# Kernel tuning notes

Hardware: AMD Instinct MI355X
Metric: run time of the kernel (lower is better)

Reference implementation:

```python
import jax, jax.numpy as jnp
import numpy as np

N_NODES = 50000
N_NEIB = 64
D = 256
BATCH = 1024
N_SAMPLES = (25, 10)  # fanout per layer (layer_specs n_sample)


def setup_inputs() -> dict:
    key = jax.random.key(0)
    ks = jax.random.split(key, 12)
    inp = {
        'ids': jax.random.randint(ks[0], (BATCH,), 0, N_NODES),
        'diff_idx': jax.random.randint(ks[1], (N_NODES, N_NEIB), 0, N_NODES),
        'diff_val': jax.random.uniform(ks[2], (N_NODES, N_NEIB), dtype=jnp.float32),
        'feats': jax.random.normal(ks[3], (N_NODES, D), dtype=jnp.float32),
    }
    # two aggregator layers, each: fc_x, fc_neib : D -> D (= output_dim//2)
    for li in range(2):
        inp[f'Wx{li+1}'] = jax.random.normal(ks[4 + 4 * li], (D, D), dtype=jnp.float32) * 0.05
        inp[f'bx{li+1}'] = jnp.zeros((D,), dtype=jnp.float32)
        inp[f'Wn{li+1}'] = jax.random.normal(ks[5 + 4 * li], (D, D), dtype=jnp.float32) * 0.05
        inp[f'bn{li+1}'] = jnp.zeros((D,), dtype=jnp.float32)
    return inp


def _sample(diff_idx, diff_val, ids, n_samples, key):
    # gather candidate neighbor rows, shared random column permutation, take first n_samples
    tmp_idx = diff_idx[ids]            # [n, N_NEIB]
    tmp_val = diff_val[ids]
    perm = jax.random.permutation(key, tmp_idx.shape[1])
    idx = tmp_idx[:, perm][:, :n_samples].reshape(-1)
    val = tmp_val[:, perm][:, :n_samples].reshape(-1)
    return idx, val


def _agg(x, neib, vals, Wx, bx, Wn, bn):
    # weighted-mean neighbor aggregation + self/neib linear combine + relu
    n = x.shape[0]
    d = neib.shape[1]
    neib = neib.reshape(n, -1, d)              # [n, s, d]
    vals = vals.reshape(n, -1)                 # [n, s]
    w = vals / (jnp.sum(vals, axis=1, keepdims=True) + 1e-10)
    m = jnp.einsum('nsd,ns->nd', neib, w)      # weighted mean of neighbors
    return jax.nn.relu(x @ Wx + bx + m @ Wn + bn)


def reference(ids, diff_idx, diff_val, feats,
              Wx1, bx1, Wn1, bn1, Wx2, bx2, Wn2, bn2):
    skey = jax.random.key(42)
    all_feats = [feats[ids]]
    all_vals = []
    cur = ids
    for li, n in enumerate(N_SAMPLES):
        cur, vals = _sample(diff_idx, diff_val, cur, n, jax.random.fold_in(skey, li))
        all_feats.append(feats[cur])
        all_vals.append(vals)
    params = [(Wx1, bx1, Wn1, bn1), (Wx2, bx2, Wn2, bn2)]
    for Wx, bx, Wn, bn in params:
        all_feats = [_agg(all_feats[k], all_feats[k + 1], all_vals[k], Wx, bx, Wn, bn)
                     for k in range(len(all_feats) - 1)]
    assert len(all_feats) == 1
    return all_feats[0]  # [BATCH, D]
```

## Files before the change

kernel.cpp:

```cpp
#include <hip/hip_runtime.h>
#include <stdint.h>
#include <stddef.h>
#include <algorithm>

#define BATCH  1024
#define S1     25
#define S2     10
#define DIM    256
#define NNEIB  64
#define L2ROWS (BATCH * S1)
#define MROWS  (BATCH + BATCH * S1)
#define KTOT   512
#define NFEAT  50000

struct Perm25 { int p[S1]; };
struct Perm10 { int p[S2]; };

typedef __attribute__((ext_vector_type(8))) short short8;
typedef __attribute__((ext_vector_type(4))) float f32x4;

static inline uint32_t rotl_(uint32_t x, int d) { return (x << d) | (x >> (32 - d)); }

static void tf2x32(uint32_t k0, uint32_t k1, uint32_t x0, uint32_t x1,
                   uint32_t* o0, uint32_t* o1) {
  const uint32_t ks0 = k0, ks1 = k1, ks2 = k0 ^ k1 ^ 0x1BD11BDAu;
  static const int R[8] = {13, 15, 26, 6, 17, 29, 16, 24};
  x0 += ks0; x1 += ks1;
  for (int g = 0; g < 5; ++g) {
    const int* rr = R + (g & 1) * 4;
    for (int i = 0; i < 4; i++) { x0 += x1; x1 = rotl_(x1, rr[i]); x1 ^= x0; }
    uint32_t a, b;
    switch (g) {
      default:
      case 0: a = ks1; b = ks2; break;
      case 1: a = ks2; b = ks0; break;
      case 2: a = ks0; b = ks1; break;
      case 3: a = ks1; b = ks2; break;
      case 4: a = ks2; b = ks0; break;
    }
    x0 += a; x1 = x1 + b + (uint32_t)(g + 1);
  }
  *o0 = x0; *o1 = x1;
}

static void compute_perm(uint32_t li, int n, int* out) {
  uint32_t k0, k1, s0, s1;
  tf2x32(0u, 42u, 0u, li, &k0, &k1);
  tf2x32(k0, k1, 0u, 1u, &s0, &s1);
  uint32_t bits[NNEIB];
  for (int i = 0; i < NNEIB; i++) {
    uint32_t a, b;
    tf2x32(s0, s1, 0u, (uint32_t)i, &a, &b);
    bits[i] = a ^ b;
  }
  int idx[NNEIB];
  for (int i = 0; i < NNEIB; i++) idx[i] = i;
  std::stable_sort(idx, idx + NNEIB, [&](int A, int B) { return bits[A] < bits[B]; });
  for (int j = 0; j < n; j++) out[j] = idx[j];
}

__device__ __forceinline__ unsigned short f2bf(float x) {
  union { float f; uint32_t u; } v; v.f = x;
  uint32_t r = (v.u + 0x7FFFu + ((v.u >> 16) & 1u)) >> 16;
  return (unsigned short)r;
}
__device__ __forceinline__ float bfbits2f(uint32_t lo16) {
  union { uint32_t u; float f; } v; v.u = lo16 << 16;
  return v.f;
}


__global__ __launch_bounds__(256) void convf_k(
    const float* __restrict__ feats, uint32_t* __restrict__ fb) {
  int i = blockIdx.x * 256 + threadIdx.x;
  f32x4 v = *(const f32x4*)&feats[(size_t)i * 4];
  uint32_t lo = f2bf(v.x) | ((uint32_t)f2bf(v.y) << 16);
  uint32_t hi = f2bf(v.z) | ((uint32_t)f2bf(v.w) << 16);
  fb[(size_t)i * 2]     = lo;
  fb[(size_t)i * 2 + 1] = hi;
}

__global__ __launch_bounds__(256) void sample1_k(
    const int* __restrict__ ids, const int* __restrict__ dix,
    const float* __restrict__ dval, int* __restrict__ growB,
    float* __restrict__ w1, Perm25 pm) {
  int i = blockIdx.x * 256 + threadIdx.x;
  if (i >= BATCH) return;
  int nid = ids[i];
  growB[i] = nid;
  const float* vr = dval + (size_t)nid * NNEIB;
  const int* ir = dix + (size_t)nid * NNEIB;
  float v[S1];
  float s = 0.f;
  for (int j = 0; j < S1; j++) { v[j] = vr[pm.p[j]]; s += v[j]; }
  float inv = 1.f / (s + 1e-10f);
  for (int j = 0; j < S1; j++) {
    w1[i * S1 + j] = v[j] * inv;
    growB[BATCH + i * S1 + j] = ir[pm.p[j]];
  }
}

__global__ __launch_bounds__(256) void sample2_k(
    const int* __restrict__ idx1, const int* __restrict__ dix,
    const float* __restrict__ dval, int* __restrict__ idx2,
    float* __restrict__ w2, Perm10 pm) {
  int p = blockIdx.x * 256 + threadIdx.x;
  if (p >= L2ROWS) return;
  int nid = idx1[p];
  const float* vr = dval + (size_t)nid * NNEIB;
  const int* ir = dix + (size_t)nid * NNEIB;
  float v[S2];
  float s = 0.f;
  for (int j = 0; j < S2; j++) { v[j] = vr[pm.p[j]]; s += v[j]; }
  float inv = 1.f / (s + 1e-10f);
  for (int j = 0; j < S2; j++) {
    w2[p * S2 + j] = v[j] * inv;
    idx2[p * S2 + j] = ir[pm.p[j]];
  }
}

__global__ __launch_bounds__(256) void stage1_k(
    const uint2* __restrict__ fb, const int* __restrict__ growB,
    const int* __restrict__ idx1, const float* __restrict__ w1,
    const int* __restrict__ idx2, const float* __restrict__ w2,
    uint2* __restrict__ A1) {
  int wave = threadIdx.x >> 6, lane = threadIdx.x & 63;
  int r = blockIdx.x * 4 + wave;
  int s;
  const int* nb;
  const float* ww;
  if (r < BATCH) { s = S1; nb = idx1 + (size_t)r * S1; ww = w1 + (size_t)r * S1; }
  else { s = S2; int b = r - BATCH; nb = idx2 + (size_t)b * S2; ww = w2 + (size_t)b * S2; }
  int nbl = 0;
  float wl = 0.f;
  if (lane < s) { nbl = nb[lane]; wl = ww[lane]; }
  int xrow = growB[r];
  A1[(size_t)r * 128 + lane] = fb[(size_t)xrow * 64 + lane];
  float a0 = 0.f, a1 = 0.f, a2 = 0.f, a3 = 0.f;
  for (int j = 0; j < s; j++) {
    int nid = __shfl(nbl, j);
    float wj = __shfl(wl, j);
    uint2 u = fb[(size_t)nid * 64 + lane];
    a0 += wj * bfbits2f(u.x & 0xffffu);
    a1 += wj * bfbits2f(u.x >> 16);
    a2 += wj * bfbits2f(u.y & 0xffffu);
    a3 += wj * bfbits2f(u.y >> 16);
  }
  uint2 o;
  o.x = f2bf(a0) | ((uint32_t)f2bf(a1) << 16);
  o.y = f2bf(a2) | ((uint32_t)f2bf(a3) << 16);
  A1[(size_t)r * 128 + 64 + lane] = o;
}

__global__ __launch_bounds__(256) void stage2_k(
    const uint2* __restrict__ Hb, const float* __restrict__ w1,
    uint2* __restrict__ A2) {
  int wave = threadIdx.x >> 6, lane = threadIdx.x & 63;
  int i = blockIdx.x * 4 + wave;
  float wl = (lane < S1) ? w1[(size_t)i * S1 + lane] : 0.f;
  A2[(size_t)i * 128 + lane] = Hb[(size_t)i * 64 + lane];
  const uint2* hb = Hb + (size_t)(BATCH + i * S1) * 64 + lane;
  float a0 = 0.f, a1 = 0.f, a2 = 0.f, a3 = 0.f;
  for (int j = 0; j < S1; j++) {
    float wj = __shfl(wl, j);
    uint2 u = hb[(size_t)j * 64];
    a0 += wj * bfbits2f(u.x & 0xffffu);
    a1 += wj * bfbits2f(u.x >> 16);
    a2 += wj * bfbits2f(u.y & 0xffffu);
    a3 += wj * bfbits2f(u.y >> 16);
  }
  uint2 o;
  o.x = f2bf(a0) | ((uint32_t)f2bf(a1) << 16);
  o.y = f2bf(a2) | ((uint32_t)f2bf(a3) << 16);
  A2[(size_t)i * 128 + 64 + lane] = o;
}

__global__ __launch_bounds__(256) void convw_k(
    const float* __restrict__ Wx, const float* __restrict__ Wn,
    unsigned short* __restrict__ Wt) {
  int idx = blockIdx.x * 256 + threadIdx.x;
  int n = idx >> 9;
  int k = idx & 511;
  float v = (k < DIM) ? Wx[(size_t)k * DIM + n] : Wn[(size_t)(k - DIM) * DIM + n];
  Wt[(size_t)n * KTOT + k] = f2bf(v);
}

#define BK 32
#define LPAD 40
template <int TBM, int TBN, bool OUT_BF16>
__global__ __launch_bounds__(256) void gemm_k(
    const unsigned short* __restrict__ A, const unsigned short* __restrict__ Wt,
    const float* __restrict__ bx, const float* __restrict__ bn,
    void* __restrict__ OutP) {
  constexpr int MI = TBM / 32;
  constexpr int NJ = TBN / 32;
  __shared__ __align__(16) unsigned short As[TBM][LPAD];
  __shared__ __align__(16) unsigned short Bs[TBN][LPAD];
  int t = threadIdx.x;
  int wave = t >> 6, lane = t & 63, quad = lane >> 4, l16 = lane & 15;
  int wm = (wave >> 1) * (TBM / 2);
  int wn = (wave & 1) * (TBN / 2);
  int row0 = blockIdx.x * TBM, col0 = blockIdx.y * TBN;

  f32x4 acc[MI][NJ];
#pragma unroll
  for (int i = 0; i < MI; i++)
#pragma unroll
    for (int j = 0; j < NJ; j++) acc[i][j] = (f32x4){0.f, 0.f, 0.f, 0.f};

  int lr = t >> 2;
  int lq = (t & 3) * 8;

  for (int k0 = 0; k0 < KTOT; k0 += BK) {
#pragma unroll
    for (int p = 0; p < TBM / 64; p++)
      *(f32x4*)&As[p * 64 + lr][lq] =
          *(const f32x4*)&A[(size_t)(row0 + p * 64 + lr) * KTOT + k0 + lq];
#pragma unroll
    for (int p = 0; p < TBN / 64; p++)
      *(f32x4*)&Bs[p * 64 + lr][lq] =
          *(const f32x4*)&Wt[(size_t)(col0 + p * 64 + lr) * KTOT + k0 + lq];
    __syncthreads();

    short8 af[MI], bfr[NJ];
#pragma unroll
    for (int i = 0; i < MI; i++)
      af[i] = *(const short8*)&As[wm + i * 16 + l16][quad * 8];
#pragma unroll
    for (int j = 0; j < NJ; j++)
      bfr[j] = *(const short8*)&Bs[wn + j * 16 + l16][quad * 8];
#pragma unroll
    for (int i = 0; i < MI; i++)
#pragma unroll
      for (int j = 0; j < NJ; j++)
        acc[i][j] = __builtin_amdgcn_mfma_f32_16x16x32_bf16(af[i], bfr[j], acc[i][j], 0, 0, 0);
    __syncthreads();
  }

  float bias[NJ];
#pragma unroll
  for (int j = 0; j < NJ; j++) {
    int c = col0 + wn + j * 16 + l16;
    bias[j] = bx[c] + bn[c];
  }
#pragma unroll
  for (int i = 0; i < MI; i++) {
#pragma unroll
    for (int j = 0; j < NJ; j++) {
      int c = col0 + wn + j * 16 + l16;
#pragma unroll
      for (int reg = 0; reg < 4; reg++) {
        int r = row0 + wm + i * 16 + quad * 4 + reg;
        float v = fmaxf(acc[i][j][reg] + bias[j], 0.f);
        if (OUT_BF16)
          ((unsigned short*)OutP)[(size_t)r * DIM + c] = f2bf(v);
        else
          ((float*)OutP)[(size_t)r * DIM + c] = v;
      }
    }
  }
}

static inline size_t align256(size_t x) { return (x + 255) & ~(size_t)255; }

extern "C" void kernel_launch(void* const* d_in, const int* in_sizes, int n_in,
                              void* d_out, int out_size, void* d_ws, size_t ws_size,
                              hipStream_t stream) {
  const int*   ids  = (const int*)d_in[0];
  const int*   dix  = (const int*)d_in[1];
  const float* dval = (const float*)d_in[2];
  const float* feats= (const float*)d_in[3];
  const float* Wx1  = (const float*)d_in[4];
  const float* bx1  = (const float*)d_in[5];
  const float* Wn1  = (const float*)d_in[6];
  const float* bn1  = (const float*)d_in[7];
  const float* Wx2  = (const float*)d_in[8];
  const float* bx2  = (const float*)d_in[9];
  const float* Wn2  = (const float*)d_in[10];
  const float* bn2  = (const float*)d_in[11];
  float* out = (float*)d_out;

  Perm25 p25;
  Perm10 p10;
  compute_perm(0u, S1, p25.p);
  compute_perm(1u, S2, p10.p);

  char* w = (char*)d_ws;
  int*            growB = (int*)w;            w += align256(sizeof(int) * MROWS);
  float*          w1    = (float*)w;          w += align256(sizeof(float) * L2ROWS);
  int*            idx2  = (int*)w;            w += align256(sizeof(int) * (size_t)L2ROWS * S2);
  float*          w2    = (float*)w;          w += align256(sizeof(float) * (size_t)L2ROWS * S2);
  uint32_t*       fb    = (uint32_t*)w;       w += align256(2 * (size_t)NFEAT * DIM);
  unsigned short* A1    = (unsigned short*)w; w += align256(2 * (size_t)MROWS * KTOT);
  unsigned short* Hb    = (unsigned short*)w; w += align256(2 * (size_t)MROWS * DIM);
  unsigned short* A2    = (unsigned short*)w; w += align256(2 * (size_t)BATCH * KTOT);
  unsigned short* Wt1   = (unsigned short*)w; w += align256(2 * (size_t)DIM * KTOT);
  unsigned short* Wt2   = (unsigned short*)w; w += align256(2 * (size_t)DIM * KTOT);
  int* idx1 = growB + BATCH;

  convf_k<<<(NFEAT * DIM / 4) / 256, 256, 0, stream>>>(feats, fb);
  convw_k<<<(DIM * KTOT) / 256, 256, 0, stream>>>(Wx1, Wn1, Wt1);
  convw_k<<<(DIM * KTOT) / 256, 256, 0, stream>>>(Wx2, Wn2, Wt2);
  sample1_k<<<(BATCH + 255) / 256, 256, 0, stream>>>(ids, dix, dval, growB, w1, p25);
  sample2_k<<<(L2ROWS + 255) / 256, 256, 0, stream>>>(idx1, dix, dval, idx2, w2, p10);
  stage1_k<<<MROWS / 4, 256, 0, stream>>>((const uint2*)fb, growB, idx1, w1, idx2, w2,
                                          (uint2*)A1);
  gemm_k<128, 128, true><<<dim3(MROWS / 128, DIM / 128), 256, 0, stream>>>(
      A1, Wt1, bx1, bn1, Hb);
  stage2_k<<<BATCH / 4, 256, 0, stream>>>((const uint2*)Hb, w1, (uint2*)A2);
  gemm_k<64, 64, false><<<dim3(BATCH / 64, DIM / 64), 256, 0, stream>>>(
      A2, Wt2, bx2, bn2, out);
}
```

Baseline: 202.2 us.

## Merge prep kernels, fold layer-2 sampling into stage1, gather self rows in GEMM

Combines the feature conversion, both weight conversions and layer-1 sampling into one prep kernel. Layer-2 sampling moves into stage1, which computes the normalized weights with a wave shuffle, so idx2/w2 are never written. The GEMMs now read the self rows straight from the bf16 feature table (or Hb) through an index, so the concatenated A matrices with their copied self halves are gone. This removes launches and intermediate traffic, at the cost of indirect row loads in the GEMM A-tile path.

```diff
diff --git a/kernel.cpp b/kernel.cpp
--- a/kernel.cpp
+++ b/kernel.cpp
@@ -70,72 +70,74 @@
 }
 
 
-__global__ __launch_bounds__(256) void convf_k(
-    const float* __restrict__ feats, uint32_t* __restrict__ fb) {
-  int i = blockIdx.x * 256 + threadIdx.x;
-  f32x4 v = *(const f32x4*)&feats[(size_t)i * 4];
-  uint32_t lo = f2bf(v.x) | ((uint32_t)f2bf(v.y) << 16);
-  uint32_t hi = f2bf(v.z) | ((uint32_t)f2bf(v.w) << 16);
-  fb[(size_t)i * 2]     = lo;
-  fb[(size_t)i * 2 + 1] = hi;
-}
-
-__global__ __launch_bounds__(256) void sample1_k(
+#define PREP_CONVF   12500
+#define PREP_CONVW   512
+#define PREP_BLOCKS  (PREP_CONVF + 2 * PREP_CONVW + 4)
+__global__ __launch_bounds__(256) void prep_k(
+    const float* __restrict__ feats, uint32_t* __restrict__ fb,
+    const float* __restrict__ Wx1, const float* __restrict__ Wn1,
+    unsigned short* __restrict__ Wt1,
+    const float* __restrict__ Wx2, const float* __restrict__ Wn2,
+    unsigned short* __restrict__ Wt2,
     const int* __restrict__ ids, const int* __restrict__ dix,
-    const float* __restrict__ dval, int* __restrict__ growB,
+    const float* __restrict__ dval, int* __restrict__ idx1,
     float* __restrict__ w1, Perm25 pm) {
-  int i = blockIdx.x * 256 + threadIdx.x;
-  if (i >= BATCH) return;
-  int nid = ids[i];
-  growB[i] = nid;
-  const float* vr = dval + (size_t)nid * NNEIB;
-  const int* ir = dix + (size_t)nid * NNEIB;
-  float v[S1];
-  float s = 0.f;
-  for (int j = 0; j < S1; j++) { v[j] = vr[pm.p[j]]; s += v[j]; }
-  float inv = 1.f / (s + 1e-10f);
-  for (int j = 0; j < S1; j++) {
-    w1[i * S1 + j] = v[j] * inv;
-    growB[BATCH + i * S1 + j] = ir[pm.p[j]];
-  }
-}
-
-__global__ __launch_bounds__(256) void sample2_k(
-    const int* __restrict__ idx1, const int* __restrict__ dix,
-    const float* __restrict__ dval, int* __restrict__ idx2,
-    float* __restrict__ w2, Perm10 pm) {
-  int p = blockIdx.x * 256 + threadIdx.x;
-  if (p >= L2ROWS) return;
-  int nid = idx1[p];
-  const float* vr = dval + (size_t)nid * NNEIB;
-  const int* ir = dix + (size_t)nid * NNEIB;
-  float v[S2];
-  float s = 0.f;
-  for (int j = 0; j < S2; j++) { v[j] = vr[pm.p[j]]; s += v[j]; }
-  float inv = 1.f / (s + 1e-10f);
-  for (int j = 0; j < S2; j++) {
-    w2[p * S2 + j] = v[j] * inv;
-    idx2[p * S2 + j] = ir[pm.p[j]];
+  int b = blockIdx.x, t = threadIdx.x;
+  if (b < PREP_CONVF) {
+    int i = b * 256 + t;
+    f32x4 v = *(const f32x4*)&feats[(size_t)i * 4];
+    fb[(size_t)i * 2]     = f2bf(v.x) | ((uint32_t)f2bf(v.y) << 16);
+    fb[(size_t)i * 2 + 1] = f2bf(v.z) | ((uint32_t)f2bf(v.w) << 16);
+  } else if (b < PREP_CONVF + 2 * PREP_CONVW) {
+    int wi = b - PREP_CONVF;
+    const float* Wx = (wi < PREP_CONVW) ? Wx1 : Wx2;
+    const float* Wn = (wi < PREP_CONVW) ? Wn1 : Wn2;
+    unsigned short* Wt = (wi < PREP_CONVW) ? Wt1 : Wt2;
+    int idx = (wi % PREP_CONVW) * 256 + t;
+    int n = idx >> 9, k = idx & 511;
+    float v = (k < DIM) ? Wx[(size_t)k * DIM + n] : Wn[(size_t)(k - DIM) * DIM + n];
+    Wt[(size_t)n * KTOT + k] = f2bf(v);
+  } else {
+    int i = (b - PREP_CONVF - 2 * PREP_CONVW) * 256 + t;
+    if (i >= BATCH) return;
+    int nid = ids[i];
+    const float* vr = dval + (size_t)nid * NNEIB;
+    const int* ir = dix + (size_t)nid * NNEIB;
+    float v[S1];
+    float s = 0.f;
+    for (int j = 0; j < S1; j++) { v[j] = vr[pm.p[j]]; s += v[j]; }
+    float inv = 1.f / (s + 1e-10f);
+    for (int j = 0; j < S1; j++) {
+      w1[i * S1 + j] = v[j] * inv;
+      idx1[i * S1 + j] = ir[pm.p[j]];
+    }
   }
 }
 
 __global__ __launch_bounds__(256) void stage1_k(
-    const uint2* __restrict__ fb, const int* __restrict__ growB,
-    const int* __restrict__ idx1, const float* __restrict__ w1,
-    const int* __restrict__ idx2, const float* __restrict__ w2,
-    uint2* __restrict__ A1) {
+    const uint2* __restrict__ fb, const int* __restrict__ idx1,
+    const float* __restrict__ w1, const int* __restrict__ dix,
+    const float* __restrict__ dval, Perm10 pm2, uint2* __restrict__ M1) {
   int wave = threadIdx.x >> 6, lane = threadIdx.x & 63;
   int r = blockIdx.x * 4 + wave;
-  int s;
-  const int* nb;
-  const float* ww;
-  if (r < BATCH) { s = S1; nb = idx1 + (size_t)r * S1; ww = w1 + (size_t)r * S1; }
-  else { s = S2; int b = r - BATCH; nb = idx2 + (size_t)b * S2; ww = w2 + (size_t)b * S2; }
-  int nbl = 0;
+  int s, nbl = 0;
   float wl = 0.f;
-  if (lane < s) { nbl = nb[lane]; wl = ww[lane]; }
-  int xrow = growB[r];
-  A1[(size_t)r * 128 + lane] = fb[(size_t)xrow * 64 + lane];
+  if (r < BATCH) {
+    s = S1;
+    if (lane < S1) { nbl = idx1[r * S1 + lane]; wl = w1[r * S1 + lane]; }
+  } else {
+    s = S2;
+    int nx = idx1[r - BATCH];
+    float vj = 0.f;
+    if (lane < S2) {
+      int c = pm2.p[lane];
+      nbl = dix[(size_t)nx * NNEIB + c];
+      vj = dval[(size_t)nx * NNEIB + c];
+    }
+    float tot = 0.f;
+    for (int j = 0; j < S2; j++) tot += __shfl(vj, j);
+    wl = vj / (tot + 1e-10f);
+  }
   float a0 = 0.f, a1 = 0.f, a2 = 0.f, a3 = 0.f;
   for (int j = 0; j < s; j++) {
     int nid = __shfl(nbl, j);
@@ -149,16 +151,15 @@
   uint2 o;
   o.x = f2bf(a0) | ((uint32_t)f2bf(a1) << 16);
   o.y = f2bf(a2) | ((uint32_t)f2bf(a3) << 16);
-  A1[(size_t)r * 128 + 64 + lane] = o;
+  M1[(size_t)r * 64 + lane] = o;
 }
 
 __global__ __launch_bounds__(256) void stage2_k(
     const uint2* __restrict__ Hb, const float* __restrict__ w1,
-    uint2* __restrict__ A2) {
+    uint2* __restrict__ M2) {
   int wave = threadIdx.x >> 6, lane = threadIdx.x & 63;
   int i = blockIdx.x * 4 + wave;
   float wl = (lane < S1) ? w1[(size_t)i * S1 + lane] : 0.f;
-  A2[(size_t)i * 128 + lane] = Hb[(size_t)i * 64 + lane];
   const uint2* hb = Hb + (size_t)(BATCH + i * S1) * 64 + lane;
   float a0 = 0.f, a1 = 0.f, a2 = 0.f, a3 = 0.f;
   for (int j = 0; j < S1; j++) {
@@ -172,26 +173,17 @@
   uint2 o;
   o.x = f2bf(a0) | ((uint32_t)f2bf(a1) << 16);
   o.y = f2bf(a2) | ((uint32_t)f2bf(a3) << 16);
-  A2[(size_t)i * 128 + 64 + lane] = o;
-}
-
-__global__ __launch_bounds__(256) void convw_k(
-    const float* __restrict__ Wx, const float* __restrict__ Wn,
-    unsigned short* __restrict__ Wt) {
-  int idx = blockIdx.x * 256 + threadIdx.x;
-  int n = idx >> 9;
-  int k = idx & 511;
-  float v = (k < DIM) ? Wx[(size_t)k * DIM + n] : Wn[(size_t)(k - DIM) * DIM + n];
-  Wt[(size_t)n * KTOT + k] = f2bf(v);
+  M2[(size_t)i * 64 + lane] = o;
 }
 
 #define BK 32
 #define LPAD 40
 template <int TBM, int TBN, bool OUT_BF16>
 __global__ __launch_bounds__(256) void gemm_k(
-    const unsigned short* __restrict__ A, const unsigned short* __restrict__ Wt,
-    const float* __restrict__ bx, const float* __restrict__ bn,
-    void* __restrict__ OutP) {
+    const unsigned short* __restrict__ Xsrc, const int* __restrict__ ids,
+    const int* __restrict__ idx1, const unsigned short* __restrict__ Mh,
+    const unsigned short* __restrict__ Wt, const float* __restrict__ bx,
+    const float* __restrict__ bn, void* __restrict__ OutP) {
   constexpr int MI = TBM / 32;
   constexpr int NJ = TBN / 32;
   __shared__ __align__(16) unsigned short As[TBM][LPAD];
@@ -210,12 +202,21 @@
 
   int lr = t >> 2;
   int lq = (t & 3) * 8;
+  int xrow[TBM / 64];
+#pragma unroll
+  for (int p = 0; p < TBM / 64; p++) {
+    int gr = row0 + p * 64 + lr;
+    xrow[p] = ids ? ((gr < BATCH) ? ids[gr] : idx1[gr - BATCH]) : gr;
+  }
 
   for (int k0 = 0; k0 < KTOT; k0 += BK) {
 #pragma unroll
-    for (int p = 0; p < TBM / 64; p++)
-      *(f32x4*)&As[p * 64 + lr][lq] =
-          *(const f32x4*)&A[(size_t)(row0 + p * 64 + lr) * KTOT + k0 + lq];
+    for (int p = 0; p < TBM / 64; p++) {
+      const unsigned short* src =
+          (k0 < DIM) ? (Xsrc + (size_t)xrow[p] * DIM + k0 + lq)
+                     : (Mh + (size_t)(row0 + p * 64 + lr) * DIM + (k0 - DIM) + lq);
+      *(f32x4*)&As[p * 64 + lr][lq] = *(const f32x4*)src;
+    }
 #pragma unroll
     for (int p = 0; p < TBN / 64; p++)
       *(f32x4*)&Bs[p * 64 + lr][lq] =
@@ -286,28 +287,22 @@
   compute_perm(1u, S2, p10.p);
 
   char* w = (char*)d_ws;
-  int*            growB = (int*)w;            w += align256(sizeof(int) * MROWS);
-  float*          w1    = (float*)w;          w += align256(sizeof(float) * L2ROWS);
-  int*            idx2  = (int*)w;            w += align256(sizeof(int) * (size_t)L2ROWS * S2);
-  float*          w2    = (float*)w;          w += align256(sizeof(float) * (size_t)L2ROWS * S2);
-  uint32_t*       fb    = (uint32_t*)w;       w += align256(2 * (size_t)NFEAT * DIM);
-  unsigned short* A1    = (unsigned short*)w; w += align256(2 * (size_t)MROWS * KTOT);
-  unsigned short* Hb    = (unsigned short*)w; w += align256(2 * (size_t)MROWS * DIM);
-  unsigned short* A2    = (unsigned short*)w; w += align256(2 * (size_t)BATCH * KTOT);
-  unsigned short* Wt1   = (unsigned short*)w; w += align256(2 * (size_t)DIM * KTOT);
-  unsigned short* Wt2   = (unsigned short*)w; w += align256(2 * (size_t)DIM * KTOT);
-  int* idx1 = growB + BATCH;
-
-  convf_k<<<(NFEAT * DIM / 4) / 256, 256, 0, stream>>>(feats, fb);
-  convw_k<<<(DIM * KTOT) / 256, 256, 0, stream>>>(Wx1, Wn1, Wt1);
-  convw_k<<<(DIM * KTOT) / 256, 256, 0, stream>>>(Wx2, Wn2, Wt2);
-  sample1_k<<<(BATCH + 255) / 256, 256, 0, stream>>>(ids, dix, dval, growB, w1, p25);
-  sample2_k<<<(L2ROWS + 255) / 256, 256, 0, stream>>>(idx1, dix, dval, idx2, w2, p10);
-  stage1_k<<<MROWS / 4, 256, 0, stream>>>((const uint2*)fb, growB, idx1, w1, idx2, w2,
-                                          (uint2*)A1);
+  int*            idx1 = (int*)w;            w += align256(sizeof(int) * L2ROWS);
+  float*          w1   = (float*)w;          w += align256(sizeof(float) * L2ROWS);
+  uint32_t*       fb   = (uint32_t*)w;       w += align256(2 * (size_t)NFEAT * DIM);
+  unsigned short* M1   = (unsigned short*)w; w += align256(2 * (size_t)MROWS * DIM);
+  unsigned short* Hb   = (unsigned short*)w; w += align256(2 * (size_t)MROWS * DIM);
+  unsigned short* M2   = (unsigned short*)w; w += align256(2 * (size_t)BATCH * DIM);
+  unsigned short* Wt1  = (unsigned short*)w; w += align256(2 * (size_t)DIM * KTOT);
+  unsigned short* Wt2  = (unsigned short*)w; w += align256(2 * (size_t)DIM * KTOT);
+
+  prep_k<<<PREP_BLOCKS, 256, 0, stream>>>(feats, fb, Wx1, Wn1, Wt1, Wx2, Wn2, Wt2,
+                                          ids, dix, dval, idx1, w1, p25);
+  stage1_k<<<MROWS / 4, 256, 0, stream>>>((const uint2*)fb, idx1, w1, dix, dval, p10,
+                                          (uint2*)M1);
   gemm_k<128, 128, true><<<dim3(MROWS / 128, DIM / 128), 256, 0, stream>>>(
-      A1, Wt1, bx1, bn1, Hb);
-  stage2_k<<<BATCH / 4, 256, 0, stream>>>((const uint2*)Hb, w1, (uint2*)A2);
+      (const unsigned short*)fb, ids, idx1, M1, Wt1, bx1, bn1, Hb);
+  stage2_k<<<BATCH / 4, 256, 0, stream>>>((const uint2*)Hb, w1, (uint2*)M2);
   gemm_k<64, 64, false><<<dim3(BATCH / 64, DIM / 64), 256, 0, stream>>>(
-      A2, Wt2, bx2, bn2, out);
-}
+      Hb, nullptr, nullptr, M2, Wt2, bx2, bn2, out);
+}
```

Measured after the change: 188.1 us (median of 2 runs). 7.0% less time.
